# Kernel tuning notes

Measured on AMD Instinct MI355X. Metric: run time of the kernel, lower is better.

The kernel has to match this reference:

```python
import jax, jax.numpy as jnp
import numpy as np

GROUP = 128  # WNA16 quantization group size along input dim


def dequant_uint4(packed, scale, zp):
    """packed: [..., K//2] int32 holding two uint4 nibbles per element.
    scale, zp: [..., K//GROUP] float. Returns [..., K] float weights."""
    lo = jnp.bitwise_and(packed, 15)
    hi = jnp.bitwise_and(jnp.right_shift(packed, 4), 15)
    q = jnp.stack([lo, hi], axis=-1).reshape(*packed.shape[:-1], -1)  # [..., K]
    K = q.shape[-1]
    qg = q.astype(scale.dtype).reshape(*q.shape[:-1], K // GROUP, GROUP)
    w = (qg - zp[..., None]) * scale[..., None]
    return w.reshape(*q.shape)


def setup_inputs() -> dict:
    key = jax.random.key(0)
    ks = jax.random.split(key, 9)
    E, T, D, I = 8, 2048, 2048, 2816
    s13 = 1.0 / (8.0 * np.sqrt(D))   # keep dequantized weights ~unit-variance scale
    s2 = 1.0 / (8.0 * np.sqrt(I))
    x = jax.random.normal(ks[0], (T, D), jnp.float32)
    topk_ids = jax.random.randint(ks[1], (T, 2), 0, E, dtype=jnp.int32)
    tw = jax.random.uniform(ks[2], (T, 2), jnp.float32) + 0.1
    topk_weights = tw / tw.sum(-1, keepdims=True)
    w13_packed = jax.random.randint(ks[3], (E, 2 * I, D // 2), 0, 256, dtype=jnp.int32)
    w13_scale = (jax.random.uniform(ks[4], (E, 2 * I, D // GROUP), jnp.float32) + 0.5) * s13
    w13_zp = jax.random.uniform(ks[5], (E, 2 * I, D // GROUP), jnp.float32) * 16.0
    w2_packed = jax.random.randint(ks[6], (E, D, I // 2), 0, 256, dtype=jnp.int32)
    w2_scale = (jax.random.uniform(ks[7], (E, D, I // GROUP), jnp.float32) + 0.5) * s2
    w2_zp = jax.random.uniform(ks[8], (E, D, I // GROUP), jnp.float32) * 16.0
    return {"x": x, "topk_ids": topk_ids, "topk_weights": topk_weights,
            "w13_packed": w13_packed, "w13_scale": w13_scale, "w13_zp": w13_zp,
            "w2_packed": w2_packed, "w2_scale": w2_scale, "w2_zp": w2_zp}


def reference(x, topk_ids, topk_weights, w13_packed, w13_scale, w13_zp,
              w2_packed, w2_scale, w2_zp):
    E = w13_packed.shape[0]
    # Dequantize per-expert int4 weights (the get_dequant_weight loop)
    W13 = dequant_uint4(w13_packed, w13_scale, w13_zp)   # [E, 2I, D]
    W2 = dequant_uint4(w2_packed, w2_scale, w2_zp)       # [E, D, I]
    # mixture_of_experts with silu activation: gate/up proj, silu-mul, down proj
    gate_up = jnp.einsum('td,eid->tei', x, W13)           # [T, E, 2I]
    g, u = jnp.split(gate_up, 2, axis=-1)
    h = jax.nn.silu(g) * u                                # [T, E, I]
    y = jnp.einsum('tei,edi->ted', h, W2)                 # [T, E, D]
    # combine top-k routed experts with router weights
    route = jnp.einsum('tke,tk->te',
                       jax.nn.one_hot(topk_ids, E, dtype=x.dtype), topk_weights)
    out = jnp.einsum('ted,te->td', y, route)              # [T, D]
    return out
```

## Files before the change

### kernel.cpp

```cpp
#include <hip/hip_runtime.h>
#include <hip/hip_bf16.h>

#define T_TOK 2048
#define DDIM  2048
#define IDIM  2816
#define NE    8
#define NPAIR (T_TOK*2)
#define GU_N  (2*IDIM)

typedef __bf16  bf16x8 __attribute__((ext_vector_type(8)));
typedef float   f32x4  __attribute__((ext_vector_type(4)));
typedef int     int4v  __attribute__((ext_vector_type(4)));
typedef unsigned int uint4v __attribute__((ext_vector_type(4)));

#define OFF_A   (64*1024)
#define OFF_GU  (OFF_A  + (size_t)NPAIR*DDIM*2)
#define OFF_H   (OFF_GU + (size_t)NPAIR*GU_N*2)
#define OFF_YP  (OFF_H  + (size_t)NPAIR*IDIM*2)

__device__ __forceinline__ unsigned short f2bf(float f) {
    __hip_bfloat16 h = __float2bfloat16(f);
    return __builtin_bit_cast(unsigned short, h);
}
__device__ __forceinline__ float bf2f(unsigned short u) {
    unsigned int x = ((unsigned int)u) << 16;
    return __builtin_bit_cast(float, x);
}
__device__ __forceinline__ unsigned int pack2bf(float lo, float hi) {
    return ((unsigned int)f2bf(hi) << 16) | (unsigned int)f2bf(lo);
}
__device__ __forceinline__ void gload_lds16(const void* g, void* l) {
    __builtin_amdgcn_global_load_lds(
        (const __attribute__((address_space(1))) void*)g,
        (__attribute__((address_space(3))) void*)l, 16, 0, 0);
}

__global__ void route_kernel(const int* __restrict__ ids, int* __restrict__ meta) {
    __shared__ int histL[NE][256];
    __shared__ int totals[NE];
    __shared__ int offsS[NE];
    const int tid = threadIdx.x;
    for (int e = 0; e < NE; ++e) histL[e][tid] = 0;
    for (int j = 0; j < 16; ++j) {
        int id = ids[tid*16 + j];
        histL[id][tid]++;
    }
    __syncthreads();
    if (tid < NE) {
        int run = 0;
        for (int i = 0; i < 256; ++i) { int v = histL[tid][i]; histL[tid][i] = run; run += v; }
        totals[tid] = run;
    }
    __syncthreads();
    if (tid == 0) {
        int run = 0;
        for (int e = 0; e < NE; ++e) {
            offsS[e] = run;
            meta[e] = totals[e];
            meta[8+e] = run;
            run += totals[e];
        }
    }
    __syncthreads();
    for (int j = 0; j < 16; ++j) {
        int p = tid*16 + j;
        int id = ids[p];
        int local = histL[id][tid];
        histL[id][tid] = local + 1;
        meta[64 + offsS[id] + local] = p;
    }
}

__global__ void gather_kernel(const float* __restrict__ x, const int* __restrict__ meta,
                              unsigned short* __restrict__ Aall) {
    const int r = blockIdx.x;
    const int p = meta[64 + r];
    const int t = p >> 1;
    const int c = threadIdx.x * 8;
    const float4* src = (const float4*)(x + (size_t)t*DDIM + c);
    float4 f0 = src[0], f1 = src[1];
    unsigned short o[8];
    o[0]=f2bf(f0.x); o[1]=f2bf(f0.y); o[2]=f2bf(f0.z); o[3]=f2bf(f0.w);
    o[4]=f2bf(f1.x); o[5]=f2bf(f1.y); o[6]=f2bf(f1.z); o[7]=f2bf(f1.w);
    int cb  = c * 2;
    int cbs = (cb & ~127) | ((cb & 127) ^ ((r & 7) << 4));
    *(uint4v*)((char*)Aall + (size_t)r*(DDIM*2) + cbs) = *(uint4v*)o;
}

#define LOADB(PK, SS, ZZ, KT)  do {                                        \
    const int4v* _bg = (const int4v*)(bgp + (KT)*32);                      \
    PK##0 = _bg[0]; PK##1 = _bg[1]; PK##2 = _bg[2]; PK##3 = _bg[3];        \
    int _g = (KT) >> 1;                                                    \
    SS = sp[_g]; ZZ = zp[_g];                                              \
} while (0)

#define ISSUE_A(SEL, KT) do {                                              \
    _Pragma("unroll")                                                      \
    for (int _i = 0; _i < 4; ++_i)                                         \
        gload_lds16(a_src[_i] + (size_t)(KT)*128,                          \
                    (char*)&As[SEL][0] + wv*4096 + _i*1024 + lane*16);     \
} while (0)

#define DEQ1(PKQ, SS, CC, BWP, QO) do {                                    \
    _Pragma("unroll")                                                      \
    for (int _j = 0; _j < 4; ++_j) {                                       \
        int _v = PKQ[_j];                                                  \
        float _lo = (float)(_v & 15);                                      \
        float _hi = (float)(_v >> 4);                                      \
        BWP[(QO)*4 + _j] = pack2bf(fmaf(_lo, SS, CC), fmaf(_hi, SS, CC));  \
    }                                                                      \
} while (0)
#define DEQ(PK, SS, ZZ, BWP) do {                                         \
    float _s = SS, _c = -(ZZ)*(SS);                                       \
    DEQ1(PK##0, _s, _c, BWP, 0); DEQ1(PK##1, _s, _c, BWP, 1);             \
    DEQ1(PK##2, _s, _c, BWP, 2); DEQ1(PK##3, _s, _c, BWP, 3);             \
} while (0)

#define WRITE_BS(BWP) do {                                                 \
    _Pragma("unroll")                                                      \
    for (int _q = 0; _q < 4; ++_q) {                                       \
        int _cb  = ahalf*64 + _q*16;                                       \
        int _cbs = _cb ^ swzB;                                             \
        *(uint4v*)(&Bs[arow*64 + (_cbs >> 1)]) = *(uint4v*)(&BWP[_q*4]);   \
    }                                                                      \
} while (0)

#define MFMA_STEP(SEL) do {                                                \
    _Pragma("unroll")                                                      \
    for (int _kk = 0; _kk < 2; ++_kk) {                                    \
        bf16x8 _af[4], _bf[4];                                             \
        const int _kbyte = _kk*64 + lk*16;                                 \
        _Pragma("unroll")                                                  \
        for (int _mi = 0; _mi < 4; ++_mi) {                                \
            int _row = wm + _mi*16 + lr;                                   \
            int _b = _kbyte ^ (((_row + base7) & 7) << 4);                 \
            _af[_mi] = *(const bf16x8*)(&As[SEL][_row*64 + (_b >> 1)]);    \
        }                                                                  \
        _Pragma("unroll")                                                  \
        for (int _nj = 0; _nj < 4; ++_nj) {                                \
            int _row = wn + _nj*16 + lr;                                   \
            int _b = _kbyte ^ ((_row & 7) << 4);                           \
            _bf[_nj] = *(const bf16x8*)(&Bs[_row*64 + (_b >> 1)]);         \
        }                                                                  \
        _Pragma("unroll")                                                  \
        for (int _mi = 0; _mi < 4; ++_mi)                                  \
            _Pragma("unroll")                                              \
            for (int _nj = 0; _nj < 4; ++_nj)                              \
                acc[_mi][_nj] = __builtin_amdgcn_mfma_f32_16x16x32_bf16(   \
                    _af[_mi], _bf[_nj], acc[_mi][_nj], 0, 0, 0);           \
    }                                                                      \
} while (0)

#define STEP(T, SELC, SELN, PKC, sC, zC, PKN, sN, zN) do {                 \
    if ((T) > 0) __syncthreads();                                          \
    int _ktn = (T)+1 < NT ? (T)+1 : NT-1;                                  \
    ISSUE_A(SELN, _ktn);                                                   \
    LOADB(PKN, sN, zN, _ktn);                                              \
    unsigned int _bw[16];                                                  \
    DEQ(PKC, sC, zC, _bw);                                                 \
    WRITE_BS(_bw);                                                         \
    __syncthreads();                                                       \
    MFMA_STEP(SELC);                                                       \
} while (0)

__launch_bounds__(256, 3)
__global__ void gemm1_kernel(const unsigned short* __restrict__ Aall,
                             const int* __restrict__ wp,
                             const float* __restrict__ wsc,
                             const float* __restrict__ wzp,
                             const int* __restrict__ meta,
                             unsigned short* __restrict__ gu) {
    const int e   = blockIdx.z;
    const int cnt = meta[e];
    const int m0  = blockIdx.y * 128;
    if (m0 >= cnt) return;
    const int off = meta[8 + e];
    const int n0  = blockIdx.x * 128;
    const int tid = threadIdx.x;

    __shared__ unsigned short As[2][128*64];
    __shared__ unsigned short Bs[128*64];

    f32x4 acc[4][4];
#pragma unroll
    for (int i = 0; i < 4; ++i)
#pragma unroll
        for (int j = 0; j < 4; ++j) acc[i][j] = (f32x4)0.0f;

    const int arow  = tid >> 1;
    const int ahalf = tid & 1;
    const int gbrow = n0 + arow;
    const int* bgp  = wp  + ((size_t)e*GU_N + gbrow)*(DDIM/2) + ahalf*16;
    const float* sp = wsc + ((size_t)e*GU_N + gbrow)*(DDIM/128);
    const float* zp = wzp + ((size_t)e*GU_N + gbrow)*(DDIM/128);
    const int swzB  = (arow & 7) << 4;

    const int lane = tid & 63;
    const int wv   = tid >> 6;
    const char* a_src[4];
#pragma unroll
    for (int i = 0; i < 4; ++i) {
        int lrow  = wv*32 + i*8 + (lane >> 3);
        int garow = off + m0 + lrow; if (garow > NPAIR-1) garow = NPAIR-1;
        a_src[i] = (const char*)Aall + (size_t)garow*(DDIM*2) + (lane & 7)*16;
    }
    const int base7 = (off + m0) & 7;

    const int wm = (wv >> 1) * 64, wn = (wv & 1) * 64;
    const int lr = lane & 15, lk = lane >> 4;

    const int NT = DDIM/64;
    int4v pkX0, pkX1, pkX2, pkX3, pkY0, pkY1, pkY2, pkY3;
    float sX, zX, sY, zY;

    ISSUE_A(0, 0);
    LOADB(pkX, sX, zX, 0);
    for (int kt = 0; kt < NT; kt += 2) {
        STEP(kt,   0, 1, pkX, sX, zX, pkY, sY, zY);
        STEP(kt+1, 1, 0, pkY, sY, zY, pkX, sX, zX);
    }

#pragma unroll
    for (int mi = 0; mi < 4; ++mi)
#pragma unroll
        for (int nj = 0; nj < 4; ++nj) {
            f32x4 v = acc[mi][nj];
            int col = n0 + wn + nj*16 + lr;
#pragma unroll
            for (int r = 0; r < 4; ++r) {
                int row = wm + mi*16 + lk*4 + r;
                if (m0 + row < cnt)
                    gu[(size_t)(off + m0 + row)*GU_N + col] = f2bf(v[r]);
            }
        }
}

__global__ void act_kernel(const unsigned short* __restrict__ gu,
                           unsigned short* __restrict__ h) {
    const int r = blockIdx.x;
    for (int c = threadIdx.x; c < IDIM/8; c += 256) {
        uint4v g8 = *(const uint4v*)(&gu[(size_t)r*GU_N + c*8]);
        uint4v u8 = *(const uint4v*)(&gu[(size_t)r*GU_N + IDIM + c*8]);
        const unsigned short* gp = (const unsigned short*)&g8;
        const unsigned short* up = (const unsigned short*)&u8;
        unsigned short o[8];
#pragma unroll
        for (int j = 0; j < 8; ++j) {
            float g = bf2f(gp[j]), u = bf2f(up[j]);
            float sg = g / (1.0f + __expf(-g));
            o[j] = f2bf(sg * u);
        }
        int cb  = c * 16;
        int cbs = (cb & ~127) | ((cb & 127) ^ ((r & 7) << 4));
        *(uint4v*)((char*)h + (size_t)r*(IDIM*2) + cbs) = *(uint4v*)o;
    }
}

__launch_bounds__(256, 3)
__global__ void gemm2_kernel(const unsigned short* __restrict__ h,
                             const int* __restrict__ wp,
                             const float* __restrict__ wsc,
                             const float* __restrict__ wzp,
                             const float* __restrict__ tw,
                             const int* __restrict__ meta,
                             float* __restrict__ yp) {
    const int e   = blockIdx.z;
    const int cnt = meta[e];
    const int m0  = blockIdx.y * 128;
    if (m0 >= cnt) return;
    const int off = meta[8 + e];
    const int n0  = blockIdx.x * 128;
    const int tid = threadIdx.x;

    __shared__ unsigned short As[2][128*64];
    __shared__ unsigned short Bs[128*64];

    f32x4 acc[4][4];
#pragma unroll
    for (int i = 0; i < 4; ++i)
#pragma unroll
        for (int j = 0; j < 4; ++j) acc[i][j] = (f32x4)0.0f;

    const int arow  = tid >> 1;
    const int ahalf = tid & 1;
    const int gbrow = n0 + arow;
    const int* bgp  = wp  + ((size_t)e*DDIM + gbrow)*(IDIM/2) + ahalf*16;
    const float* sp = wsc + ((size_t)e*DDIM + gbrow)*(IDIM/128);
    const float* zp = wzp + ((size_t)e*DDIM + gbrow)*(IDIM/128);
    const int swzB  = (arow & 7) << 4;

    const int lane = tid & 63;
    const int wv   = tid >> 6;
    const char* a_src[4];
#pragma unroll
    for (int i = 0; i < 4; ++i) {
        int lrow  = wv*32 + i*8 + (lane >> 3);
        int garow = off + m0 + lrow; if (garow > NPAIR-1) garow = NPAIR-1;
        a_src[i] = (const char*)h + (size_t)garow*(IDIM*2) + (lane & 7)*16;
    }
    const int base7 = (off + m0) & 7;

    const int wm = (wv >> 1) * 64, wn = (wv & 1) * 64;
    const int lr = lane & 15, lk = lane >> 4;

    const int NT = IDIM/64;
    int4v pkX0, pkX1, pkX2, pkX3, pkY0, pkY1, pkY2, pkY3;
    float sX, zX, sY, zY;

    ISSUE_A(0, 0);
    LOADB(pkX, sX, zX, 0);
    for (int kt = 0; kt < NT; kt += 2) {
        STEP(kt,   0, 1, pkX, sX, zX, pkY, sY, zY);
        STEP(kt+1, 1, 0, pkY, sY, zY, pkX, sX, zX);
    }

#pragma unroll
    for (int mi = 0; mi < 4; ++mi)
#pragma unroll
        for (int nj = 0; nj < 4; ++nj) {
            f32x4 v = acc[mi][nj];
            int col = n0 + wn + nj*16 + lr;
#pragma unroll
            for (int r = 0; r < 4; ++r) {
                int row = wm + mi*16 + lk*4 + r;
                if (m0 + row < cnt) {
                    int p = meta[64 + off + m0 + row];
                    float w = tw[p];
                    yp[(size_t)p*DDIM + col] = v[r] * w;
                }
            }
        }
}

__global__ void combine_kernel(const float* __restrict__ yp, float* __restrict__ out) {
    const int i = blockIdx.x * 256 + threadIdx.x;
    const int t = i >> 9, d = i & 511;
    const f32x4* a = (const f32x4*)yp;
    f32x4 va = a[(size_t)(t*2)*512 + d];
    f32x4 vb = a[(size_t)(t*2+1)*512 + d];
    ((f32x4*)out)[i] = va + vb;
}

extern "C" void kernel_launch(void* const* d_in, const int* in_sizes, int n_in,
                              void* d_out, int out_size, void* d_ws, size_t ws_size,
                              hipStream_t stream) {
    const float* x    = (const float*)d_in[0];
    const int*   ids  = (const int*)d_in[1];
    const float* tw   = (const float*)d_in[2];
    const int*   w13p = (const int*)d_in[3];
    const float* w13s = (const float*)d_in[4];
    const float* w13z = (const float*)d_in[5];
    const int*   w2p  = (const int*)d_in[6];
    const float* w2s  = (const float*)d_in[7];
    const float* w2z  = (const float*)d_in[8];
    float* out = (float*)d_out;

    char* ws = (char*)d_ws;
    int* meta = (int*)ws;
    unsigned short* Aall = (unsigned short*)(ws + OFF_A);
    unsigned short* gu   = (unsigned short*)(ws + OFF_GU);
    unsigned short* h    = (unsigned short*)(ws + OFF_H);
    float* yp            = (float*)(ws + OFF_YP);

    route_kernel<<<1, 256, 0, stream>>>(ids, meta);
    gather_kernel<<<NPAIR, 256, 0, stream>>>(x, meta, Aall);
    gemm1_kernel<<<dim3(GU_N/128, NPAIR/128, NE), 256, 0, stream>>>(Aall, w13p, w13s, w13z, meta, gu);
    act_kernel<<<NPAIR, 256, 0, stream>>>(gu, h);
    gemm2_kernel<<<dim3(DDIM/128, NPAIR/128, NE), 256, 0, stream>>>(h, w2p, w2s, w2z, tw, meta, yp);
    combine_kernel<<<(T_TOK*DDIM/4)/256, 256, 0, stream>>>(yp, out);
}
```

Measured before the change: 376.6 us.

## Double-buffer dequantized B tile and drop per-step barrier in MoE GEMMs

```diff
diff --git a/kernel.cpp b/kernel.cpp
--- a/kernel.cpp
+++ b/kernel.cpp
@@ -116,16 +116,16 @@
     DEQ1(PK##2, _s, _c, BWP, 2); DEQ1(PK##3, _s, _c, BWP, 3);             \
 } while (0)
 
-#define WRITE_BS(BWP) do {                                                 \
+#define WRITE_BS(BWP, BSEL) do {                                           \
     _Pragma("unroll")                                                      \
     for (int _q = 0; _q < 4; ++_q) {                                       \
         int _cb  = ahalf*64 + _q*16;                                       \
         int _cbs = _cb ^ swzB;                                             \
-        *(uint4v*)(&Bs[arow*64 + (_cbs >> 1)]) = *(uint4v*)(&BWP[_q*4]);   \
+        *(uint4v*)(&Bs[BSEL][arow*64 + (_cbs >> 1)]) = *(uint4v*)(&BWP[_q*4]); \
     }                                                                      \
 } while (0)
 
-#define MFMA_STEP(SEL) do {                                                \
+#define MFMA_STEP(ASEL, BSEL) do {                                         \
     _Pragma("unroll")                                                      \
     for (int _kk = 0; _kk < 2; ++_kk) {                                    \
         bf16x8 _af[4], _bf[4];                                             \
@@ -134,13 +134,13 @@
         for (int _mi = 0; _mi < 4; ++_mi) {                                \
             int _row = wm + _mi*16 + lr;                                   \
             int _b = _kbyte ^ (((_row + base7) & 7) << 4);                 \
-            _af[_mi] = *(const bf16x8*)(&As[SEL][_row*64 + (_b >> 1)]);    \
+            _af[_mi] = *(const bf16x8*)(&As[ASEL][_row*64 + (_b >> 1)]);   \
         }                                                                  \
         _Pragma("unroll")                                                  \
         for (int _nj = 0; _nj < 4; ++_nj) {                                \
             int _row = wn + _nj*16 + lr;                                   \
             int _b = _kbyte ^ ((_row & 7) << 4);                           \
-            _bf[_nj] = *(const bf16x8*)(&Bs[_row*64 + (_b >> 1)]);         \
+            _bf[_nj] = *(const bf16x8*)(&Bs[BSEL][_row*64 + (_b >> 1)]);   \
         }                                                                  \
         _Pragma("unroll")                                                  \
         for (int _mi = 0; _mi < 4; ++_mi)                                  \
@@ -151,19 +151,18 @@
     }                                                                      \
 } while (0)
 
-#define STEP(T, SELC, SELN, PKC, sC, zC, PKN, sN, zN) do {                 \
-    if ((T) > 0) __syncthreads();                                          \
-    int _ktn = (T)+1 < NT ? (T)+1 : NT-1;                                  \
-    ISSUE_A(SELN, _ktn);                                                   \
-    LOADB(PKN, sN, zN, _ktn);                                              \
+#define STEP1(T, AS_CUR, AS_NXT, PKC, sC, zC, PKN, sN, zN) do {            \
     unsigned int _bw[16];                                                  \
     DEQ(PKC, sC, zC, _bw);                                                 \
-    WRITE_BS(_bw);                                                         \
+    WRITE_BS(_bw, (T) & 1);                                                \
     __syncthreads();                                                       \
-    MFMA_STEP(SELC);                                                       \
-} while (0)
-
-__launch_bounds__(256, 3)
+    int _ktn = (T)+1 < NT ? (T)+1 : NT-1;                                  \
+    ISSUE_A(AS_NXT, _ktn);                                                 \
+    LOADB(PKN, sN, zN, _ktn);                                              \
+    MFMA_STEP(AS_CUR, (T) & 1);                                            \
+} while (0)
+
+__launch_bounds__(256, 2)
 __global__ void gemm1_kernel(const unsigned short* __restrict__ Aall,
                              const int* __restrict__ wp,
                              const float* __restrict__ wsc,
@@ -179,7 +178,7 @@
     const int tid = threadIdx.x;
 
     __shared__ unsigned short As[2][128*64];
-    __shared__ unsigned short Bs[128*64];
+    __shared__ unsigned short Bs[2][128*64];
 
     f32x4 acc[4][4];
 #pragma unroll
@@ -216,9 +215,10 @@
     ISSUE_A(0, 0);
     LOADB(pkX, sX, zX, 0);
     for (int kt = 0; kt < NT; kt += 2) {
-        STEP(kt,   0, 1, pkX, sX, zX, pkY, sY, zY);
-        STEP(kt+1, 1, 0, pkY, sY, zY, pkX, sX, zX);
-    }
+        STEP1(kt,   0, 1, pkX, sX, zX, pkY, sY, zY);
+        STEP1(kt+1, 1, 0, pkY, sY, zY, pkX, sX, zX);
+    }
+    __syncthreads();
 
 #pragma unroll
     for (int mi = 0; mi < 4; ++mi)
@@ -256,7 +256,7 @@
     }
 }
 
-__launch_bounds__(256, 3)
+__launch_bounds__(256, 2)
 __global__ void gemm2_kernel(const unsigned short* __restrict__ h,
                              const int* __restrict__ wp,
                              const float* __restrict__ wsc,
@@ -273,7 +273,7 @@
     const int tid = threadIdx.x;
 
     __shared__ unsigned short As[2][128*64];
-    __shared__ unsigned short Bs[128*64];
+    __shared__ unsigned short Bs[2][128*64];
 
     f32x4 acc[4][4];
 #pragma unroll
@@ -310,9 +310,10 @@
     ISSUE_A(0, 0);
     LOADB(pkX, sX, zX, 0);
     for (int kt = 0; kt < NT; kt += 2) {
-        STEP(kt,   0, 1, pkX, sX, zX, pkY, sY, zY);
-        STEP(kt+1, 1, 0, pkY, sY, zY, pkX, sX, zX);
-    }
+        STEP1(kt,   0, 1, pkX, sX, zX, pkY, sY, zY);
+        STEP1(kt+1, 1, 0, pkY, sY, zY, pkX, sX, zX);
+    }
+    __syncthreads();
 
 #pragma unroll
     for (int mi = 0; mi < 4; ++mi)
```

Measured after the change: 488.5 us. +29.7%, slower.

## Repack int32-per-byte weights into dense uint32 before each GEMM

Applied to the files above, without the earlier changes.

```diff
diff --git a/kernel.cpp b/kernel.cpp
--- a/kernel.cpp
+++ b/kernel.cpp
@@ -17,6 +17,8 @@
 #define OFF_GU  (OFF_A  + (size_t)NPAIR*DDIM*2)
 #define OFF_H   (OFF_GU + (size_t)NPAIR*GU_N*2)
 #define OFF_YP  (OFF_H  + (size_t)NPAIR*IDIM*2)
+#define W13_DWORDS (NE*(size_t)GU_N*(DDIM/8))
+#define W2_DWORDS  (NE*(size_t)DDIM*(IDIM/8))
 
 __device__ __forceinline__ unsigned short f2bf(float f) {
     __hip_bfloat16 h = __float2bfloat16(f);
@@ -87,9 +89,20 @@
     *(uint4v*)((char*)Aall + (size_t)r*(DDIM*2) + cbs) = *(uint4v*)o;
 }
 
+__global__ void repack_kernel(const int* __restrict__ src,
+                              unsigned int* __restrict__ dst, int nwords) {
+    const int i = blockIdx.x * 256 + threadIdx.x;
+    if (i >= nwords) return;
+    int4v p = *(const int4v*)(src + (size_t)i*4);
+    unsigned int d = ((unsigned int)p[0] & 0xFFu)
+                   | (((unsigned int)p[1] & 0xFFu) << 8)
+                   | (((unsigned int)p[2] & 0xFFu) << 16)
+                   | (((unsigned int)p[3] & 0xFFu) << 24);
+    dst[i] = d;
+}
+
 #define LOADB(PK, SS, ZZ, KT)  do {                                        \
-    const int4v* _bg = (const int4v*)(bgp + (KT)*32);                      \
-    PK##0 = _bg[0]; PK##1 = _bg[1]; PK##2 = _bg[2]; PK##3 = _bg[3];        \
+    PK = *(const uint4v*)(bgp + (size_t)(KT)*8);                           \
     int _g = (KT) >> 1;                                                    \
     SS = sp[_g]; ZZ = zp[_g];                                              \
 } while (0)
@@ -101,19 +114,18 @@
                     (char*)&As[SEL][0] + wv*4096 + _i*1024 + lane*16);     \
 } while (0)
 
-#define DEQ1(PKQ, SS, CC, BWP, QO) do {                                    \
+#define DEQ(PK, SS, ZZ, BWP) do {                                          \
+    float _s = SS, _c = -(ZZ)*(SS);                                        \
     _Pragma("unroll")                                                      \
-    for (int _j = 0; _j < 4; ++_j) {                                       \
-        int _v = PKQ[_j];                                                  \
-        float _lo = (float)(_v & 15);                                      \
-        float _hi = (float)(_v >> 4);                                      \
-        BWP[(QO)*4 + _j] = pack2bf(fmaf(_lo, SS, CC), fmaf(_hi, SS, CC));  \
+    for (int _q = 0; _q < 4; ++_q) {                                       \
+        unsigned int _w = PK[_q];                                          \
+        _Pragma("unroll")                                                  \
+        for (int _j = 0; _j < 4; ++_j) {                                   \
+            float _lo = (float)((_w >> (8*_j)) & 15u);                     \
+            float _hi = (float)((_w >> (8*_j + 4)) & 15u);                 \
+            BWP[_q*4 + _j] = pack2bf(fmaf(_lo, _s, _c), fmaf(_hi, _s, _c));\
+        }                                                                  \
     }                                                                      \
-} while (0)
-#define DEQ(PK, SS, ZZ, BWP) do {                                         \
-    float _s = SS, _c = -(ZZ)*(SS);                                       \
-    DEQ1(PK##0, _s, _c, BWP, 0); DEQ1(PK##1, _s, _c, BWP, 1);             \
-    DEQ1(PK##2, _s, _c, BWP, 2); DEQ1(PK##3, _s, _c, BWP, 3);             \
 } while (0)
 
 #define WRITE_BS(BWP) do {                                                 \
@@ -165,7 +177,7 @@
 
 __launch_bounds__(256, 3)
 __global__ void gemm1_kernel(const unsigned short* __restrict__ Aall,
-                             const int* __restrict__ wp,
+                             const unsigned int* __restrict__ wd,
                              const float* __restrict__ wsc,
                              const float* __restrict__ wzp,
                              const int* __restrict__ meta,
@@ -190,7 +202,7 @@
     const int arow  = tid >> 1;
     const int ahalf = tid & 1;
     const int gbrow = n0 + arow;
-    const int* bgp  = wp  + ((size_t)e*GU_N + gbrow)*(DDIM/2) + ahalf*16;
+    const unsigned int* bgp = wd + ((size_t)e*GU_N + gbrow)*(DDIM/8) + ahalf*4;
     const float* sp = wsc + ((size_t)e*GU_N + gbrow)*(DDIM/128);
     const float* zp = wzp + ((size_t)e*GU_N + gbrow)*(DDIM/128);
     const int swzB  = (arow & 7) << 4;
@@ -210,7 +222,7 @@
     const int lr = lane & 15, lk = lane >> 4;
 
     const int NT = DDIM/64;
-    int4v pkX0, pkX1, pkX2, pkX3, pkY0, pkY1, pkY2, pkY3;
+    uint4v pkX, pkY;
     float sX, zX, sY, zY;
 
     ISSUE_A(0, 0);
@@ -258,7 +270,7 @@
 
 __launch_bounds__(256, 3)
 __global__ void gemm2_kernel(const unsigned short* __restrict__ h,
-                             const int* __restrict__ wp,
+                             const unsigned int* __restrict__ wd,
                              const float* __restrict__ wsc,
                              const float* __restrict__ wzp,
                              const float* __restrict__ tw,
@@ -284,7 +296,7 @@
     const int arow  = tid >> 1;
     const int ahalf = tid & 1;
     const int gbrow = n0 + arow;
-    const int* bgp  = wp  + ((size_t)e*DDIM + gbrow)*(IDIM/2) + ahalf*16;
+    const unsigned int* bgp = wd + ((size_t)e*DDIM + gbrow)*(IDIM/8) + ahalf*4;
     const float* sp = wsc + ((size_t)e*DDIM + gbrow)*(IDIM/128);
     const float* zp = wzp + ((size_t)e*DDIM + gbrow)*(IDIM/128);
     const int swzB  = (arow & 7) << 4;
@@ -304,7 +316,7 @@
     const int lr = lane & 15, lk = lane >> 4;
 
     const int NT = IDIM/64;
-    int4v pkX0, pkX1, pkX2, pkX3, pkY0, pkY1, pkY2, pkY3;
+    uint4v pkX, pkY;
     float sX, zX, sY, zY;
 
     ISSUE_A(0, 0);
@@ -361,11 +373,15 @@
     unsigned short* gu   = (unsigned short*)(ws + OFF_GU);
     unsigned short* h    = (unsigned short*)(ws + OFF_H);
     float* yp            = (float*)(ws + OFF_YP);
+    unsigned int* W13d = (unsigned int*)(ws + OFF_H);
+    unsigned int* W2d  = (unsigned int*)(ws + OFF_GU);
 
     route_kernel<<<1, 256, 0, stream>>>(ids, meta);
     gather_kernel<<<NPAIR, 256, 0, stream>>>(x, meta, Aall);
-    gemm1_kernel<<<dim3(GU_N/128, NPAIR/128, NE), 256, 0, stream>>>(Aall, w13p, w13s, w13z, meta, gu);
+    repack_kernel<<<(int)(W13_DWORDS/256), 256, 0, stream>>>(w13p, W13d, (int)W13_DWORDS);
+    gemm1_kernel<<<dim3(GU_N/128, NPAIR/128, NE), 256, 0, stream>>>(Aall, W13d, w13s, w13z, meta, gu);
     act_kernel<<<NPAIR, 256, 0, stream>>>(gu, h);
-    gemm2_kernel<<<dim3(DDIM/128, NPAIR/128, NE), 256, 0, stream>>>(h, w2p, w2s, w2z, tw, meta, yp);
+    repack_kernel<<<(int)(W2_DWORDS/256), 256, 0, stream>>>(w2p, W2d, (int)W2_DWORDS);
+    gemm2_kernel<<<dim3(DDIM/128, NPAIR/128, NE), 256, 0, stream>>>(h, W2d, w2s, w2z, tw, meta, yp);
     combine_kernel<<<(T_TOK*DDIM/4)/256, 256, 0, stream>>>(yp, out);
 }
```

Result: no change. 380.4 us (+1.0%).

## Split int4 dequantization into separate chunked kernels feeding plain bf16 GEMMs

Applied to the files above, without the earlier changes.

```diff
diff --git a/kernel.cpp b/kernel.cpp
--- a/kernel.cpp
+++ b/kernel.cpp
@@ -7,6 +7,11 @@
 #define NE    8
 #define NPAIR (T_TOK*2)
 #define GU_N  (2*IDIM)
+
+#define CH13  1408
+#define NCH13 4
+#define CH2   1024
+#define NCH2  2
 
 typedef __bf16  bf16x8 __attribute__((ext_vector_type(8)));
 typedef float   f32x4  __attribute__((ext_vector_type(4)));
@@ -87,45 +92,73 @@
     *(uint4v*)((char*)Aall + (size_t)r*(DDIM*2) + cbs) = *(uint4v*)o;
 }
 
-#define LOADB(PK, SS, ZZ, KT)  do {                                        \
-    const int4v* _bg = (const int4v*)(bgp + (KT)*32);                      \
-    PK##0 = _bg[0]; PK##1 = _bg[1]; PK##2 = _bg[2]; PK##3 = _bg[3];        \
-    int _g = (KT) >> 1;                                                    \
-    SS = sp[_g]; ZZ = zp[_g];                                              \
-} while (0)
-
-#define ISSUE_A(SEL, KT) do {                                              \
+__global__ void deq13_kernel(const int* __restrict__ wp,
+                             const float* __restrict__ wsc,
+                             const float* __restrict__ wzp,
+                             unsigned short* __restrict__ Wb, int row0) {
+    const int lrow = blockIdx.x;
+    const int e    = blockIdx.y;
+    const int r    = row0 + lrow;
+    const int c    = threadIdx.x;
+    int4v p = *(const int4v*)(wp + ((size_t)e*GU_N + r)*(DDIM/2) + c*4);
+    const int g = c >> 4;
+    float s  = wsc[((size_t)e*GU_N + r)*(DDIM/128) + g];
+    float z  = wzp[((size_t)e*GU_N + r)*(DDIM/128) + g];
+    float cc = -z*s;
+    unsigned int o[4];
+#pragma unroll
+    for (int j = 0; j < 4; ++j) {
+        int v = p[j];
+        float lo = (float)(v & 15);
+        float hi = (float)((v >> 4) & 15);
+        o[j] = pack2bf(fmaf(lo, s, cc), fmaf(hi, s, cc));
+    }
+    int cb  = c * 16;
+    int cbs = (cb & ~127) | ((cb & 127) ^ ((lrow & 7) << 4));
+    *(uint4v*)((char*)Wb + ((size_t)e*CH13 + lrow)*(DDIM*2) + cbs) = *(uint4v*)o;
+}
+
+__global__ void deq2_kernel(const int* __restrict__ wp,
+                            const float* __restrict__ wsc,
+                            const float* __restrict__ wzp,
+                            unsigned short* __restrict__ Wb, int row0) {
+    const int lrow = blockIdx.x;
+    const int e    = blockIdx.y;
+    const int r    = row0 + lrow;
+    for (int c = threadIdx.x; c < IDIM/8; c += 256) {
+        int4v p = *(const int4v*)(wp + ((size_t)e*DDIM + r)*(IDIM/2) + c*4);
+        const int g = c >> 4;
+        float s  = wsc[((size_t)e*DDIM + r)*(IDIM/128) + g];
+        float z  = wzp[((size_t)e*DDIM + r)*(IDIM/128) + g];
+        float cc = -z*s;
+        unsigned int o[4];
+#pragma unroll
+        for (int j = 0; j < 4; ++j) {
+            int v = p[j];
+            float lo = (float)(v & 15);
+            float hi = (float)((v >> 4) & 15);
+            o[j] = pack2bf(fmaf(lo, s, cc), fmaf(hi, s, cc));
+        }
+        int cb  = c * 16;
+        int cbs = (cb & ~127) | ((cb & 127) ^ ((lrow & 7) << 4));
+        *(uint4v*)((char*)Wb + ((size_t)e*CH2 + lrow)*(IDIM*2) + cbs) = *(uint4v*)o;
+    }
+}
+
+#define ISSUE_A(KT) do {                                                   \
     _Pragma("unroll")                                                      \
     for (int _i = 0; _i < 4; ++_i)                                         \
         gload_lds16(a_src[_i] + (size_t)(KT)*128,                          \
-                    (char*)&As[SEL][0] + wv*4096 + _i*1024 + lane*16);     \
+                    (char*)As + wv*4096 + _i*1024 + lane*16);              \
 } while (0)
-
-#define DEQ1(PKQ, SS, CC, BWP, QO) do {                                    \
+#define ISSUE_B(KT) do {                                                   \
     _Pragma("unroll")                                                      \
-    for (int _j = 0; _j < 4; ++_j) {                                       \
-        int _v = PKQ[_j];                                                  \
-        float _lo = (float)(_v & 15);                                      \
-        float _hi = (float)(_v >> 4);                                      \
-        BWP[(QO)*4 + _j] = pack2bf(fmaf(_lo, SS, CC), fmaf(_hi, SS, CC));  \
-    }                                                                      \
+    for (int _i = 0; _i < 4; ++_i)                                         \
+        gload_lds16(b_src[_i] + (size_t)(KT)*128,                          \
+                    (char*)Bs + wv*4096 + _i*1024 + lane*16);              \
 } while (0)
-#define DEQ(PK, SS, ZZ, BWP) do {                                         \
-    float _s = SS, _c = -(ZZ)*(SS);                                       \
-    DEQ1(PK##0, _s, _c, BWP, 0); DEQ1(PK##1, _s, _c, BWP, 1);             \
-    DEQ1(PK##2, _s, _c, BWP, 2); DEQ1(PK##3, _s, _c, BWP, 3);             \
-} while (0)
-
-#define WRITE_BS(BWP) do {                                                 \
-    _Pragma("unroll")                                                      \
-    for (int _q = 0; _q < 4; ++_q) {                                       \
-        int _cb  = ahalf*64 + _q*16;                                       \
-        int _cbs = _cb ^ swzB;                                             \
-        *(uint4v*)(&Bs[arow*64 + (_cbs >> 1)]) = *(uint4v*)(&BWP[_q*4]);   \
-    }                                                                      \
-} while (0)
-
-#define MFMA_STEP(SEL) do {                                                \
+
+#define MFMA_STEP() do {                                                   \
     _Pragma("unroll")                                                      \
     for (int _kk = 0; _kk < 2; ++_kk) {                                    \
         bf16x8 _af[4], _bf[4];                                             \
@@ -134,7 +167,7 @@
         for (int _mi = 0; _mi < 4; ++_mi) {                                \
             int _row = wm + _mi*16 + lr;                                   \
             int _b = _kbyte ^ (((_row + base7) & 7) << 4);                 \
-            _af[_mi] = *(const bf16x8*)(&As[SEL][_row*64 + (_b >> 1)]);    \
+            _af[_mi] = *(const bf16x8*)(&As[_row*64 + (_b >> 1)]);         \
         }                                                                  \
         _Pragma("unroll")                                                  \
         for (int _nj = 0; _nj < 4; ++_nj) {                                \
@@ -151,34 +184,20 @@
     }                                                                      \
 } while (0)
 
-#define STEP(T, SELC, SELN, PKC, sC, zC, PKN, sN, zN) do {                 \
-    if ((T) > 0) __syncthreads();                                          \
-    int _ktn = (T)+1 < NT ? (T)+1 : NT-1;                                  \
-    ISSUE_A(SELN, _ktn);                                                   \
-    LOADB(PKN, sN, zN, _ktn);                                              \
-    unsigned int _bw[16];                                                  \
-    DEQ(PKC, sC, zC, _bw);                                                 \
-    WRITE_BS(_bw);                                                         \
-    __syncthreads();                                                       \
-    MFMA_STEP(SELC);                                                       \
-} while (0)
-
 __launch_bounds__(256, 3)
 __global__ void gemm1_kernel(const unsigned short* __restrict__ Aall,
-                             const int* __restrict__ wp,
-                             const float* __restrict__ wsc,
-                             const float* __restrict__ wzp,
+                             const unsigned short* __restrict__ Wb,
                              const int* __restrict__ meta,
-                             unsigned short* __restrict__ gu) {
+                             unsigned short* __restrict__ gu, int col0) {
     const int e   = blockIdx.z;
     const int cnt = meta[e];
     const int m0  = blockIdx.y * 128;
     if (m0 >= cnt) return;
     const int off = meta[8 + e];
-    const int n0  = blockIdx.x * 128;
+    const int bx  = blockIdx.x;
     const int tid = threadIdx.x;
 
-    __shared__ unsigned short As[2][128*64];
+    __shared__ unsigned short As[128*64];
     __shared__ unsigned short Bs[128*64];
 
     f32x4 acc[4][4];
@@ -186,23 +205,18 @@
     for (int i = 0; i < 4; ++i)
 #pragma unroll
         for (int j = 0; j < 4; ++j) acc[i][j] = (f32x4)0.0f;
-
-    const int arow  = tid >> 1;
-    const int ahalf = tid & 1;
-    const int gbrow = n0 + arow;
-    const int* bgp  = wp  + ((size_t)e*GU_N + gbrow)*(DDIM/2) + ahalf*16;
-    const float* sp = wsc + ((size_t)e*GU_N + gbrow)*(DDIM/128);
-    const float* zp = wzp + ((size_t)e*GU_N + gbrow)*(DDIM/128);
-    const int swzB  = (arow & 7) << 4;
 
     const int lane = tid & 63;
     const int wv   = tid >> 6;
     const char* a_src[4];
+    const char* b_src[4];
 #pragma unroll
     for (int i = 0; i < 4; ++i) {
         int lrow  = wv*32 + i*8 + (lane >> 3);
         int garow = off + m0 + lrow; if (garow > NPAIR-1) garow = NPAIR-1;
         a_src[i] = (const char*)Aall + (size_t)garow*(DDIM*2) + (lane & 7)*16;
+        b_src[i] = (const char*)Wb +
+                   ((size_t)e*CH13 + bx*128 + lrow)*(DDIM*2) + (lane & 7)*16;
     }
     const int base7 = (off + m0) & 7;
 
@@ -210,14 +224,12 @@
     const int lr = lane & 15, lk = lane >> 4;
 
     const int NT = DDIM/64;
-    int4v pkX0, pkX1, pkX2, pkX3, pkY0, pkY1, pkY2, pkY3;
-    float sX, zX, sY, zY;
-
-    ISSUE_A(0, 0);
-    LOADB(pkX, sX, zX, 0);
-    for (int kt = 0; kt < NT; kt += 2) {
-        STEP(kt,   0, 1, pkX, sX, zX, pkY, sY, zY);
-        STEP(kt+1, 1, 0, pkY, sY, zY, pkX, sX, zX);
+    for (int kt = 0; kt < NT; ++kt) {
+        if (kt > 0) __syncthreads();
+        ISSUE_A(kt);
+        ISSUE_B(kt);
+        __syncthreads();
+        MFMA_STEP();
     }
 
 #pragma unroll
@@ -225,7 +237,7 @@
 #pragma unroll
         for (int nj = 0; nj < 4; ++nj) {
             f32x4 v = acc[mi][nj];
-            int col = n0 + wn + nj*16 + lr;
+            int col = col0 + bx*128 + wn + nj*16 + lr;
 #pragma unroll
             for (int r = 0; r < 4; ++r) {
                 int row = wm + mi*16 + lk*4 + r;
@@ -258,21 +270,19 @@
 
 __launch_bounds__(256, 3)
 __global__ void gemm2_kernel(const unsigned short* __restrict__ h,
-                             const int* __restrict__ wp,
-                             const float* __restrict__ wsc,
-                             const float* __restrict__ wzp,
+                             const unsigned short* __restrict__ Wb,
                              const float* __restrict__ tw,
                              const int* __restrict__ meta,
-                             float* __restrict__ yp) {
+                             float* __restrict__ yp, int col0) {
     const int e   = blockIdx.z;
     const int cnt = meta[e];
     const int m0  = blockIdx.y * 128;
     if (m0 >= cnt) return;
     const int off = meta[8 + e];
-    const int n0  = blockIdx.x * 128;
+    const int bx  = blockIdx.x;
     const int tid = threadIdx.x;
 
-    __shared__ unsigned short As[2][128*64];
+    __shared__ unsigned short As[128*64];
     __shared__ unsigned short Bs[128*64];
 
     f32x4 acc[4][4];
@@ -280,23 +290,18 @@
     for (int i = 0; i < 4; ++i)
 #pragma unroll
         for (int j = 0; j < 4; ++j) acc[i][j] = (f32x4)0.0f;
-
-    const int arow  = tid >> 1;
-    const int ahalf = tid & 1;
-    const int gbrow = n0 + arow;
-    const int* bgp  = wp  + ((size_t)e*DDIM + gbrow)*(IDIM/2) + ahalf*16;
-    const float* sp = wsc + ((size_t)e*DDIM + gbrow)*(IDIM/128);
-    const float* zp = wzp + ((size_t)e*DDIM + gbrow)*(IDIM/128);
-    const int swzB  = (arow & 7) << 4;
 
     const int lane = tid & 63;
     const int wv   = tid >> 6;
     const char* a_src[4];
+    const char* b_src[4];
 #pragma unroll
     for (int i = 0; i < 4; ++i) {
         int lrow  = wv*32 + i*8 + (lane >> 3);
         int garow = off + m0 + lrow; if (garow > NPAIR-1) garow = NPAIR-1;
         a_src[i] = (const char*)h + (size_t)garow*(IDIM*2) + (lane & 7)*16;
+        b_src[i] = (const char*)Wb +
+                   ((size_t)e*CH2 + bx*128 + lrow)*(IDIM*2) + (lane & 7)*16;
     }
     const int base7 = (off + m0) & 7;
 
@@ -304,14 +309,12 @@
     const int lr = lane & 15, lk = lane >> 4;
 
     const int NT = IDIM/64;
-    int4v pkX0, pkX1, pkX2, pkX3, pkY0, pkY1, pkY2, pkY3;
-    float sX, zX, sY, zY;
-
-    ISSUE_A(0, 0);
-    LOADB(pkX, sX, zX, 0);
-    for (int kt = 0; kt < NT; kt += 2) {
-        STEP(kt,   0, 1, pkX, sX, zX, pkY, sY, zY);
-        STEP(kt+1, 1, 0, pkY, sY, zY, pkX, sX, zX);
+    for (int kt = 0; kt < NT; ++kt) {
+        if (kt > 0) __syncthreads();
+        ISSUE_A(kt);
+        ISSUE_B(kt);
+        __syncthreads();
+        MFMA_STEP();
     }
 
 #pragma unroll
@@ -319,7 +322,7 @@
 #pragma unroll
         for (int nj = 0; nj < 4; ++nj) {
             f32x4 v = acc[mi][nj];
-            int col = n0 + wn + nj*16 + lr;
+            int col = col0 + bx*128 + wn + nj*16 + lr;
 #pragma unroll
             for (int r = 0; r < 4; ++r) {
                 int row = wm + mi*16 + lk*4 + r;
@@ -361,11 +364,21 @@
     unsigned short* gu   = (unsigned short*)(ws + OFF_GU);
     unsigned short* h    = (unsigned short*)(ws + OFF_H);
     float* yp            = (float*)(ws + OFF_YP);
+    unsigned short* W13b = (unsigned short*)(ws + OFF_H);
+    unsigned short* W2b  = (unsigned short*)(ws + OFF_GU);
 
     route_kernel<<<1, 256, 0, stream>>>(ids, meta);
     gather_kernel<<<NPAIR, 256, 0, stream>>>(x, meta, Aall);
-    gemm1_kernel<<<dim3(GU_N/128, NPAIR/128, NE), 256, 0, stream>>>(Aall, w13p, w13s, w13z, meta, gu);
+    for (int c = 0; c < NCH13; ++c) {
+        deq13_kernel<<<dim3(CH13, NE), 256, 0, stream>>>(w13p, w13s, w13z, W13b, c*CH13);
+        gemm1_kernel<<<dim3(CH13/128, NPAIR/128, NE), 256, 0, stream>>>(
+            Aall, W13b, meta, gu, c*CH13);
+    }
     act_kernel<<<NPAIR, 256, 0, stream>>>(gu, h);
-    gemm2_kernel<<<dim3(DDIM/128, NPAIR/128, NE), 256, 0, stream>>>(h, w2p, w2s, w2z, tw, meta, yp);
+    for (int c = 0; c < NCH2; ++c) {
+        deq2_kernel<<<dim3(CH2, NE), 256, 0, stream>>>(w2p, w2s, w2z, W2b, c*CH2);
+        gemm2_kernel<<<dim3(CH2/128, NPAIR/128, NE), 256, 0, stream>>>(
+            h, W2b, tw, meta, yp, c*CH2);
+    }
     combine_kernel<<<(T_TOK*DDIM/4)/256, 256, 0, stream>>>(yp, out);
 }
```

New measurement: 538.6 us. +43.0%, slower.
